# Kernel optimization log

Measured on AMD Instinct MI355X. Metric: run time of the kernel, lower is better.

The kernel has to match this reference:

```python
import jax, jax.numpy as jnp
import numpy as np
import math

C64 = jnp.complex64

def _fftconv_full(a, kern):
    # full linear convolution along last axis (complex), like scipy.signal.fftconvolve
    L = a.shape[-1] + kern.shape[0] - 1
    A = jnp.fft.fft(a, n=L, axis=-1)
    K = jnp.fft.fft(kern.astype(a.dtype), n=L)
    return jnp.fft.ifft(A * K, axis=-1)

def _centered_ifft(f):
    # out[shft] = ifft(f[shft]) * sqrt(N), shft = (arange(N)+fix(N/2)) % N
    N = f.shape[-1]
    shft = (np.arange(N) + int(np.fix(N / 2))) % N
    inv = np.argsort(shft)
    g = jnp.fft.ifft(f[..., shft], axis=-1) * math.sqrt(N)
    return g[..., inv].astype(f.dtype)

def _sincinterp(f):
    # zero-stuff by 2 then sinc-filter; returns length 2N-1 along last axis
    N = f.shape[-1]
    y = jnp.zeros(f.shape[:-1] + (2 * N - 1,), f.dtype).at[..., ::2].set(f)
    kern = jnp.asarray(np.sinc(np.arange(-(2 * N - 3), 2 * N - 2) / 2.0).astype(np.complex64))
    return _fftconv_full(y, kern)[..., 2 * N - 3: 4 * N - 4]

def _frft_chirp(f, a):
    # Ozaktas chirp-convolution discrete FrFT, valid for 0.5 <= a <= 1.5
    N = f.shape[-1]
    alpha = a * math.pi / 2
    tana2, sina = math.tan(alpha / 2), math.sin(alpha)
    fi = _sincinterp(f)                                   # [..., 2N-1]
    pad = jnp.zeros(f.shape[:-1] + (N - 1,), f.dtype)
    fp = jnp.concatenate([pad, fi, pad], axis=-1)         # [..., 4N-3]
    n = np.arange(-2 * N + 2, 2 * N - 1).astype(np.float64)
    chrp = jnp.asarray(np.exp(-1j * math.pi / N * tana2 / 4 * n ** 2).astype(np.complex64))
    fp = chrp * fp
    c = math.pi / N / sina / 4
    m = np.arange(-(4 * N - 4), 4 * N - 3).astype(np.float64)
    kern = jnp.asarray(np.exp(1j * c * m ** 2).astype(np.complex64))
    ret = _fftconv_full(fp, kern)[..., 4 * N - 4: 8 * N - 7] * math.sqrt(c / math.pi)
    ret = chrp * ret
    phase = np.complex64(np.exp(-1j * (1 - a) * math.pi / 4))
    return phase * ret[..., N - 1: 3 * N - 2: 2]          # [..., N]

def _frft_last(f, a):
    # torch branch logic for the a values used here: a=0.5 (fwd), a=-0.5 (inv)
    if a < 0.5:
        f = _centered_ifft(f)
        a = a + 1.0
    return _frft_chirp(f, a)

def _frft2d(x, a):
    t = _frft_last(x, a)                                  # rows: along W
    return jnp.swapaxes(_frft_last(jnp.swapaxes(t, -1, -2), a), -1, -2)  # cols: along H

def _c1x1(x, w, b=None):
    y = jnp.einsum('nchw,oc->nohw', x, w)
    return y if b is None else y + b[None, :, None, None]

def _c3x3(x, w, b):
    y = jax.lax.conv_general_dilated(x, w, (1, 1), 'SAME',
                                     dimension_numbers=('NCHW', 'OIHW', 'NCHW'))
    return y + b[None, :, None, None]

def _forward(x, conv1_w, mag_s_w, mag_s_b, mag_f_w, mag_f_b, mag_w, mag_b,
             pha_w, pha_b, conv_0_w, conv_0_b, conv_1_w, conv_1_b, conv2_w):
    angle = 0.5
    alpha = math.cos(angle * math.pi / 2)
    N, C, H, W = x.shape
    H1, W1 = int(H * alpha), int(W * alpha)
    x1 = _c1x1(x, conv1_w)                                # stride=1 -> downsample is identity
    C1, C0 = C // 4, C // 4 // 3
    x_0, x_05, x_1 = x1[:, :C0], x1[:, C0:C1 - C0], x1[:, C1 - C0:C1]
    h0, w0 = (H - H1) // 2, (W - W1) // 2
    mask1 = jnp.zeros((H, W), jnp.float32).at[h0:h0 + H1, w0:w0 + W1].set(1.0)
    mask2 = 1.0 - mask1
    # fractional Fourier branch
    Fre = _frft2d(x_05.astype(C64), angle)
    mag, pha = jnp.abs(Fre), jnp.angle(Fre)
    mag_out = _c1x1(_c3x3(mag * mask1, mag_s_w, mag_s_b) * mask1
                    + _c1x1(mag * mask2, mag_f_w, mag_f_b) * mask2, mag_w, mag_b)
    pha_out = _c1x1(pha, pha_w, pha_b)
    Fre_out = jax.lax.complex(mag_out * jnp.cos(pha_out), mag_out * jnp.sin(pha_out))
    ifrft = jnp.abs(_frft2d(Fre_out, -angle))
    # plain Fourier branch (conv_1 applied to both mag and pha, as in the source)
    fre = jnp.fft.rfft2(x_1)
    fm, fp = jnp.abs(fre), jnp.angle(fre)
    mo = _c1x1(fm, conv_1_w, conv_1_b)
    po = _c1x1(fp, conv_1_w, conv_1_b)
    x_1o = jnp.fft.irfft2(jax.lax.complex(mo * jnp.cos(po), mo * jnp.sin(po)), s=(H, W))
    x_0o = _c1x1(x_0, conv_0_w, conv_0_b)
    return _c1x1(jnp.concatenate([x_0o, ifrft, x_1o], axis=1), conv2_w)

def setup_inputs():
    key = jax.random.key(0)
    ks = jax.random.split(key, 16)
    N, C, H, W, Co = 4, 192, 128, 128, 192
    C1, C0 = C // 4, C // 4 // 3
    Cm = C1 - 2 * C0
    s = 0.05
    r = lambda k, sh: jax.random.normal(k, sh, jnp.float32)
    return {
        "x": r(ks[0], (N, C, H, W)),
        "conv1_w": r(ks[1], (C1, C)) * s,
        "mag_s_w": r(ks[2], (Cm, Cm, 3, 3)) * s, "mag_s_b": r(ks[3], (Cm,)) * s,
        "mag_f_w": r(ks[4], (Cm, Cm)) * s, "mag_f_b": r(ks[5], (Cm,)) * s,
        "mag_w": r(ks[6], (Cm, Cm)) * s, "mag_b": r(ks[7], (Cm,)) * s,
        "pha_w": r(ks[8], (Cm, Cm)) * s, "pha_b": r(ks[9], (Cm,)) * s,
        "conv_0_w": r(ks[10], (C0, C0)) * s, "conv_0_b": r(ks[11], (C0,)) * s,
        "conv_1_w": r(ks[12], (C0, C0)) * s, "conv_1_b": r(ks[13], (C0,)) * s,
        "conv2_w": r(ks[14], (Co, C1)) * s,
    }

def reference(x, conv1_w, mag_s_w, mag_s_b, mag_f_w, mag_f_b, mag_w, mag_b,
              pha_w, pha_b, conv_0_w, conv_0_b, conv_1_w, conv_1_b, conv2_w):
    return _forward(x, conv1_w, mag_s_w, mag_s_b, mag_f_w, mag_f_b, mag_w, mag_b,
                    pha_w, pha_b, conv_0_w, conv_0_b, conv_1_w, conv_1_b, conv2_w)
```

## Files before the change

kernel.cpp:

```cpp
#include <hip/hip_runtime.h>
#include <math.h>

#define PI_D 3.14159265358979323846
#define TWO_PI_F 6.2831853071795864f

__device__ __align__(16) float2 g_Mf [128*128];
__device__ __align__(16) float2 g_MfT[128*128];
__device__ __align__(16) float2 g_Mb [128*128];
__device__ __align__(16) float2 g_MbT[128*128];
__device__ __align__(16) float2 g_F  [128*128];
__device__ __align__(16) float2 g_IF [128*128];
__device__ __align__(16) float  g_x1 [4*48*16384];
__device__ __align__(16) float2 g_bufA[64*16384];
__device__ __align__(16) float2 g_bufB[64*16384];
__device__ __align__(16) float  g_mag[64*16384];
__device__ __align__(16) float  g_pha[64*16384];
__device__ __align__(16) float  g_m65[64*8320];
__device__ __align__(16) float  g_p65[64*8320];
__device__ __align__(16) float  g_t1 [64*16384];
__device__ __align__(16) float  g_t2 [64*16384];
__device__ __align__(16) float  g_t3 [64*8320];
__device__ __align__(16) float  g_t4 [64*8320];
__device__ __align__(16) float  g_cat[4*48*16384];

__device__ inline void build_A_body(int tid) {
    if (tid >= 128*128) return;
    int o = tid >> 7, m = tid & 127;
    const double chc = -PI_D/128.0 * tan(PI_D/8.0) * 0.25;
    const double c   =  PI_D/(512.0*sin(PI_D/4.0));
    const double inv2pi = 1.0/(2.0*PI_D);
    float sr, si;
    {
        int n1 = 2*m - 127, tt = 2*(o - m);
        double ang = chc*(double)(n1*n1) + c*(double)(tt*tt);
        double r = ang*inv2pi; r -= floor(r);
        float af = (float)(r*2.0*PI_D);
        float sn, cs; __sincosf(af, &sn, &cs);
        sr = cs; si = sn;
    }
    for (int j = 0; j < 127; ++j) {
        int q  = 2*j + 1;
        int n1 = q - 127, tt = 2*o - q, d = q - 2*m;
        double ang = chc*(double)(n1*n1) + c*(double)(tt*tt);
        double r = ang*inv2pi; r -= floor(r);
        float af = (float)(r*2.0*PI_D);
        float s = (((d-1)>>1) & 1) ? -2.0f : 2.0f;
        s /= (3.14159265358979f*(float)d);
        float sn, cs; __sincosf(af, &sn, &cs);
        sr += s*cs; si += s*sn;
    }
    int n2 = 2*o - 127;
    double ph = chc*(double)(n2*n2) - PI_D/8.0;
    double r = ph*inv2pi; r -= floor(r);
    float pf = (float)(r*2.0*PI_D);
    float scale = (float)sqrt(c/PI_D);
    float sn, cs; __sincosf(pf, &sn, &cs);
    float cr = cs*scale, ci = sn*scale;
    float2 v = make_float2(sr*cr - si*ci, sr*ci + si*cr);
    g_Mf[tid] = v;
    g_MfT[(m<<7) + o] = v;
    int p = (o*m) & 127;
    float ang2 = TWO_PI_F*(float)p/128.0f;
    float sn2, cs2; __sincosf(ang2, &sn2, &cs2);
    g_F[tid]  = make_float2(cs2, -sn2);
    g_IF[tid] = make_float2(cs2*0.0078125f, sn2*0.0078125f);
}

template<int LM>
__device__ inline void load_T4(float2* tr, const float* mp, const float* pp,
                               const float* Trl, int hh, int w4) {
    if (LM == 2) {
#pragma unroll
        for (int i = 0; i < 4; ++i) {
            int idx = (hh<<7) + w4 + i;
            float m = mp[idx], ph = pp[idx];
            float sn, cs; __sincosf(ph, &sn, &cs);
            tr[i] = make_float2(m*cs, m*sn);
        }
    } else {
#pragma unroll
        for (int i = 0; i < 4; ++i) {
            int w = w4 + i;
            int h2 = hh, w2 = w; float sg = 1.f;
            if (w >= 65) { h2 = (128 - hh) & 127; w2 = 128 - w; sg = -1.f; }
            int idx = h2*65 + w2;
            float m = mp[idx], ph = pp[idx];
            float sn, cs; __sincosf(ph, &sn, &cs);
            tr[i] = make_float2(m*cs, sg*m*sn);
        }
    }
}

__device__ inline void cfma(float2& a, float sx, float sy, float mx, float my) {
    a.x = fmaf(sx, mx, a.x); a.x = fmaf(-sy, my, a.x);
    a.y = fmaf(sx, my, a.y); a.y = fmaf(sy, mx, a.y);
}

template<int LM>
__device__ inline void rmul_body(const float2* __restrict__ MT, const float* __restrict__ Trl,
                                 const float* __restrict__ mp_, const float* __restrict__ pp_,
                                 float2* __restrict__ out, int cstart,
                                 int p, int r0, int t, float2* Ssh) {
    constexpr bool RS = (LM == 1);
    const float* Trp = nullptr; const float* mp = nullptr; const float* pp = nullptr;
    if (LM == 1) { int n = p >> 4, c = p & 15; Trp = Trl + ((long)(n*48 + cstart + c) << 14); }
    if (LM == 2) { mp = mp_ + ((long)p << 14); pp = pp_ + ((long)p << 14); }
    if (LM == 3) { mp = mp_ + (long)p*8320;   pp = pp_ + (long)p*8320; }
    int cq = t & 63, rp = t >> 6;
    const float* Tr_row[4];
    if (RS) {
#pragma unroll
        for (int i = 0; i < 4; ++i) {
            int ro = __builtin_amdgcn_readfirstlane((r0 + (rp<<2) + i) << 7);
            Tr_row[i] = Trp + ro;
        }
    } else {
        for (int u = t; u < 512; u += 256) {
            int row = u >> 5, w4 = (u & 31) << 2;
            float2 tr4[4];
            load_T4<LM>(tr4, mp, pp, Trp, r0 + row, w4);
            float4* d = (float4*)&Ssh[(row << 7) + w4];
            d[0] = make_float4(tr4[0].x, tr4[0].y, tr4[1].x, tr4[1].y);
            d[1] = make_float4(tr4[2].x, tr4[2].y, tr4[3].x, tr4[3].y);
        }
        __syncthreads();
    }
    float2 acc[4][2] = {};
#pragma unroll 8
    for (int k2 = 0; k2 < 64; ++k2) {
        int k = k2 << 1;
        float4 m0 = *(const float4*)&MT[(k << 7) + (cq<<1)];
        float4 m1 = *(const float4*)&MT[((k+1) << 7) + (cq<<1)];
        if (RS) {
            float2 sr4[4];
#pragma unroll
            for (int i = 0; i < 4; ++i)
                sr4[i] = *(const float2*)(Tr_row[i] + k);
#pragma unroll
            for (int i = 0; i < 4; ++i) {
                acc[i][0].x = fmaf(sr4[i].x, m0.x, acc[i][0].x);
                acc[i][0].y = fmaf(sr4[i].x, m0.y, acc[i][0].y);
                acc[i][1].x = fmaf(sr4[i].x, m0.z, acc[i][1].x);
                acc[i][1].y = fmaf(sr4[i].x, m0.w, acc[i][1].y);
                acc[i][0].x = fmaf(sr4[i].y, m1.x, acc[i][0].x);
                acc[i][0].y = fmaf(sr4[i].y, m1.y, acc[i][0].y);
                acc[i][1].x = fmaf(sr4[i].y, m1.z, acc[i][1].x);
                acc[i][1].y = fmaf(sr4[i].y, m1.w, acc[i][1].y);
            }
        } else {
            float4 s2[4];
#pragma unroll
            for (int i = 0; i < 4; ++i)
                s2[i] = *(const float4*)&Ssh[(((rp<<2)+i) << 7) + k];
#pragma unroll
            for (int i = 0; i < 4; ++i) {
                cfma(acc[i][0], s2[i].x, s2[i].y, m0.x, m0.y);
                cfma(acc[i][1], s2[i].x, s2[i].y, m0.z, m0.w);
                cfma(acc[i][0], s2[i].z, s2[i].w, m1.x, m1.y);
                cfma(acc[i][1], s2[i].z, s2[i].w, m1.z, m1.w);
            }
        }
    }
    long base = ((long)p << 14);
#pragma unroll
    for (int i = 0; i < 4; ++i) {
        float4* dst = (float4*)(out + base + ((long)(r0 + (rp<<2) + i) << 7) + (cq<<1));
        *dst = make_float4(acc[i][0].x, acc[i][0].y, acc[i][1].x, acc[i][1].y);
    }
}

template<int EPI>
__device__ inline void lmul_body(const float2* __restrict__ A, const float2* __restrict__ in,
                                 float* __restrict__ o1, float* __restrict__ o2, int coff,
                                 int p, int j0, int t) {
    const float2* T = in + ((long)p << 14);
    int cq = t & 63, rp = t >> 6;
    const float2* Arow[4];
#pragma unroll
    for (int i = 0; i < 4; ++i) {
        int ro = __builtin_amdgcn_readfirstlane((j0 + (rp<<2) + i) << 7);
        Arow[i] = A + ro;
    }
    float2 acc[4][2] = {};
#pragma unroll 8
    for (int k2 = 0; k2 < 64; ++k2) {
        int k = k2 << 1;
        float4 m0 = *(const float4*)&T[(k << 7) + (cq<<1)];
        float4 m1 = *(const float4*)&T[((k+1) << 7) + (cq<<1)];
        float4 s2[4];
#pragma unroll
        for (int i = 0; i < 4; ++i)
            s2[i] = *(const float4*)(Arow[i] + k);
#pragma unroll
        for (int i = 0; i < 4; ++i) {
            if (EPI == 3) {
                acc[i][0].x = fmaf(s2[i].x, m0.x, acc[i][0].x);
                acc[i][0].x = fmaf(-s2[i].y, m0.y, acc[i][0].x);
                acc[i][1].x = fmaf(s2[i].x, m0.z, acc[i][1].x);
                acc[i][1].x = fmaf(-s2[i].y, m0.w, acc[i][1].x);
                acc[i][0].x = fmaf(s2[i].z, m1.x, acc[i][0].x);
                acc[i][0].x = fmaf(-s2[i].w, m1.y, acc[i][0].x);
                acc[i][1].x = fmaf(s2[i].z, m1.z, acc[i][1].x);
                acc[i][1].x = fmaf(-s2[i].w, m1.w, acc[i][1].x);
            } else {
                cfma(acc[i][0], s2[i].x, s2[i].y, m0.x, m0.y);
                cfma(acc[i][1], s2[i].x, s2[i].y, m0.z, m0.w);
                cfma(acc[i][0], s2[i].z, s2[i].w, m1.x, m1.y);
                cfma(acc[i][1], s2[i].z, s2[i].w, m1.z, m1.w);
            }
        }
    }
#pragma unroll
    for (int i = 0; i < 4; ++i) {
        int jj = j0 + (rp<<2) + i;
        int ww0 = cq << 1;
        float2 v0 = acc[i][0], v1 = acc[i][1];
        if (EPI == 1) {
            long idx = ((long)p << 14) + ((long)jj << 7) + ww0;
            *(float2*)&o1[idx] = make_float2(sqrtf(v0.x*v0.x + v0.y*v0.y),
                                             sqrtf(v1.x*v1.x + v1.y*v1.y));
            *(float2*)&o2[idx] = make_float2(atan2f(v0.y, v0.x), atan2f(v1.y, v1.x));
        } else if (EPI == 2) {
            int n = p >> 4, c = p & 15;
            long idx = ((long)(n*48 + coff + c) << 14) + ((long)jj << 7) + ww0;
            *(float2*)&o1[idx] = make_float2(sqrtf(v0.x*v0.x + v0.y*v0.y),
                                             sqrtf(v1.x*v1.x + v1.y*v1.y));
        } else if (EPI == 3) {
            int n = p >> 4, c = p & 15;
            long idx = ((long)(n*48 + coff + c) << 14) + ((long)jj << 7) + ww0;
            *(float2*)&o1[idx] = make_float2(v0.x, v1.x);
        } else if (EPI == 4) {
            if (ww0 < 65) {
                long idx = (long)p*8320 + jj*65 + ww0;
                o1[idx] = sqrtf(v0.x*v0.x + v0.y*v0.y);
                o2[idx] = atan2f(v0.y, v0.x);
                if (ww0 + 1 < 65) {
                    o1[idx+1] = sqrtf(v1.x*v1.x + v1.y*v1.y);
                    o2[idx+1] = atan2f(v1.y, v1.x);
                }
            }
        }
    }
}

template<int LMA, int LMB>
__global__ __launch_bounds__(256, 4)
void k_rmul_dual(const float2* __restrict__ MTa, const float* __restrict__ TrlA,
                 const float* __restrict__ mpA, const float* __restrict__ ppA,
                 float2* __restrict__ outA, int cstartA,
                 const float2* __restrict__ MTb, const float* __restrict__ TrlB,
                 const float* __restrict__ mpB, const float* __restrict__ ppB,
                 float2* __restrict__ outB, int cstartB) {
    __shared__ __align__(16) float2 Ssh[(LMA == 1 && LMB == 1) ? 2 : 16*128];
    __shared__ float2 W[128];
    int bx = blockIdx.x, by = blockIdx.y, t = threadIdx.x;
    if (bx >= 128) {
        int b = (bx - 128)*8 + by;
        if (b < 64) {
            if (t < 128) {
                float ang = TWO_PI_F*(float)t/128.0f;
                float sn, cs; __sincosf(ang, &sn, &cs);
                float invs = 0.08838834764831845f;
                W[t] = make_float2(cs*invs, sn*invs);
            }
            __syncthreads();
            int tid = b*256 + t;
            int o = tid >> 7, m = tid & 127;
            float sr = 0.f, si = 0.f;
            for (int r = 0; r < 128; ++r) {
                float2 a = g_Mf[(o<<7) + r];
                int k = ((r+64)*(m+64)) & 127;
                float2 w = W[k];
                sr += a.x*w.x - a.y*w.y;
                si += a.x*w.y + a.y*w.x;
            }
            float2 v = make_float2(sr, si);
            g_Mb[tid] = v;
            g_MbT[(m<<7) + o] = v;
        }
        return;
    }
    int p = bx & 63, r0 = by << 4;
    if (bx < 64) rmul_body<LMA>(MTa, TrlA, mpA, ppA, outA, cstartA, p, r0, t, Ssh);
    else         rmul_body<LMB>(MTb, TrlB, mpB, ppB, outB, cstartB, p, r0, t, Ssh);
}

template<int EPIA, int EPIB>
__global__ __launch_bounds__(256, 4)
void k_lmul_dual(const float2* __restrict__ Aa, const float2* __restrict__ inA,
                 float* __restrict__ o1A, float* __restrict__ o2A, int coffA,
                 const float2* __restrict__ Ab, const float2* __restrict__ inB,
                 float* __restrict__ o1B, float* __restrict__ o2B, int coffB) {
    int bx = blockIdx.x, j0 = blockIdx.y << 4, t = threadIdx.x;
    int p = bx & 63;
    if (bx < 64) lmul_body<EPIA>(Aa, inA, o1A, o2A, coffA, p, j0, t);
    else         lmul_body<EPIB>(Ab, inB, o1B, o2B, coffB, p, j0, t);
}

template<int CIN, int COUT, int KSPLIT, int OSPLIT>
__device__ inline void wconv_body(const float* __restrict__ in, const float* __restrict__ wgt,
                                  const float* __restrict__ bias, float* __restrict__ out,
                                  int S, int Ctin, int cstart, int Ctout, int costart,
                                  int n, int sblk, float* red) {
    constexpr int OW = COUT / OSPLIT;
    constexpr int KC = CIN / KSPLIT;
    int t = threadIdx.x, lane = t & 63;
    int wv = __builtin_amdgcn_readfirstlane(t >> 6);
    int oq = wv / KSPLIT, kq = wv % KSPLIT;
    int s0 = sblk << 7;
    const float* inb = in + ((long)(n*Ctin + cstart + kq*KC))*S + s0 + (lane<<1);
    const float* wb  = wgt + (oq*OW)*CIN + kq*KC;
    float2 acc[OW];
#pragma unroll
    for (int j = 0; j < OW; ++j) acc[j] = make_float2(0.f, 0.f);
#pragma unroll 4
    for (int c = 0; c < KC; ++c) {
        float2 xv = *(const float2*)(inb + (long)c*S);
#pragma unroll
        for (int j = 0; j < OW; ++j) {
            float w = wb[j*CIN + c];
            acc[j].x = fmaf(w, xv.x, acc[j].x);
            acc[j].y = fmaf(w, xv.y, acc[j].y);
        }
    }
    if (KSPLIT == 1) {
#pragma unroll
        for (int j = 0; j < OW; ++j) {
            int o = oq*OW + j;
            float b = bias ? bias[o] : 0.f;
            *(float2*)(out + ((long)(n*Ctout + costart + o))*S + s0 + (lane<<1))
                = make_float2(acc[j].x + b, acc[j].y + b);
        }
    } else {
#pragma unroll
        for (int j = 0; j < OW; ++j) {
            int o = oq*OW + j;
            *(float2*)&red[((kq*COUT + o) << 7) + (lane<<1)] = acc[j];
        }
        __syncthreads();
        for (int idx = t; idx < COUT*64; idx += 256) {
            int o = idx >> 6, l2 = (idx & 63) << 1;
            float b = bias ? bias[o] : 0.f;
            float2 v = make_float2(b, b);
#pragma unroll
            for (int k2 = 0; k2 < KSPLIT; ++k2) {
                float2 r = *(const float2*)&red[((k2*COUT + o) << 7) + l2];
                v.x += r.x; v.y += r.y;
            }
            *(float2*)(out + ((long)(n*Ctout + costart + o))*S + s0 + l2) = v;
        }
    }
}

__global__ __launch_bounds__(256, 1)
void k_conv1_build(const float* __restrict__ x, const float* __restrict__ w,
                   float* __restrict__ x1) {
    __shared__ float red[2*48*128];
    if (blockIdx.z == 0) {
        wconv_body<192,48,2,2>(x, w, nullptr, x1, 16384, 192, 0, 48, 0,
                               blockIdx.y, blockIdx.x, red);
    } else {
        int b = blockIdx.y*gridDim.x + blockIdx.x;
        if (b < 64) build_A_body(b*256 + threadIdx.x);
    }
}

__global__ __launch_bounds__(256, 1)
void k_conv2(const float* __restrict__ in, const float* __restrict__ wgt,
             float* __restrict__ out) {
    __shared__ float red[1];
    wconv_body<48,192,1,4>(in, wgt, nullptr, out, 16384, 48, 0, 192, 0,
                           blockIdx.y, blockIdx.x, red);
}

__device__ inline void mix16b(const float* __restrict__ in, const float* __restrict__ w,
                              const float* __restrict__ b, float* __restrict__ out,
                              int Ctin, int S, int n, int s0base, int Slim) {
    int t = threadIdx.x, lane = t & 63;
    int wv = __builtin_amdgcn_readfirstlane(t >> 6);
    int oq = wv & 3, pg = wv >> 2;
    int s0 = s0base + (pg << 7);
    if (s0 >= Slim) return;
    const float* inb = in + ((long)(n*Ctin))*S + s0 + (lane<<1);
    float2 acc[4];
#pragma unroll
    for (int j = 0; j < 4; ++j) {
        float bb = b ? b[oq*4 + j] : 0.f;
        acc[j] = make_float2(bb, bb);
    }
#pragma unroll
    for (int half = 0; half < 2; ++half) {
        float2 xv[8];
#pragma unroll
        for (int c = 0; c < 8; ++c)
            xv[c] = *(const float2*)(inb + (long)(half*8 + c)*S);
#pragma unroll
        for (int c = 0; c < 8; ++c) {
#pragma unroll
            for (int j = 0; j < 4; ++j) {
                float ww = w[(oq*4 + j)*16 + half*8 + c];
                acc[j].x = fmaf(ww, xv[c].x, acc[j].x);
                acc[j].y = fmaf(ww, xv[c].y, acc[j].y);
            }
        }
    }
#pragma unroll
    for (int j = 0; j < 4; ++j) {
        int o = oq*4 + j;
        *(float2*)(out + ((long)(n*Ctin + o))*S + s0 + (lane<<1)) = acc[j];
    }
}

__device__ inline void maskconv_body(const float* __restrict__ mag, const float* __restrict__ ws3,
                                     const float* __restrict__ bs, const float* __restrict__ wf,
                                     const float* __restrict__ bf, const float* __restrict__ wm,
                                     const float* __restrict__ bm, float* __restrict__ out,
                                     int n, int tile, float* patch) {
    int h0 = (tile >> 3) << 4, w0 = (tile & 7) << 4;
    int t = threadIdx.x;
    const float* magn = mag + ((long)n << 18);
    for (int idx = t; idx < 16*324; idx += 1024) {
        int c = idx / 324, r = idx - c*324;
        int ph = r / 18, pw = r - ph*18;
        int gh = h0 - 1 + ph, gw = w0 - 1 + pw;
        float v = 0.f;
        if (gh >= 19 && gh < 109 && gw >= 19 && gw < 109)
            v = magn[(c<<14) + (gh<<7) + gw];
        patch[c*324 + r] = v;
    }
    __syncthreads();
    int oq = t >> 8, pix = t & 255;
    int ty = pix >> 4, tx = pix & 15;
    int h = h0 + ty, w = w0 + tx;
    bool in1 = (h >= 19 && h < 109 && w >= 19 && w < 109);
    unsigned long long bal = __ballot(in1);
    float res[4];
    if (bal != 0ull) {
        float acc[4];
#pragma unroll
        for (int j = 0; j < 4; ++j) acc[j] = bs[oq*4 + j];
        for (int c = 0; c < 16; ++c) {
            const float* pc = patch + c*324 + ty*18 + tx;
            const float* wc = ws3 + c*9;
#pragma unroll
            for (int dh = 0; dh < 3; ++dh) {
#pragma unroll
                for (int dw = 0; dw < 3; ++dw) {
                    float tap = pc[dh*18 + dw];
#pragma unroll
                    for (int j = 0; j < 4; ++j)
                        acc[j] = fmaf(wc[(oq*4 + j)*144 + dh*3 + dw], tap, acc[j]);
                }
            }
        }
#pragma unroll
        for (int j = 0; j < 4; ++j) res[j] = acc[j];
    }
    if (bal != ~0ull) {
        float acc2[4];
#pragma unroll
        for (int j = 0; j < 4; ++j) acc2[j] = bf[oq*4 + j];
#pragma unroll
        for (int half = 0; half < 2; ++half) {
            float xv[8];
#pragma unroll
            for (int c = 0; c < 8; ++c)
                xv[c] = magn[((half*8 + c)<<14) + (h<<7) + w];
#pragma unroll
            for (int c = 0; c < 8; ++c)
#pragma unroll
                for (int j = 0; j < 4; ++j)
                    acc2[j] = fmaf(wf[(oq*4 + j)*16 + half*8 + c], xv[c], acc2[j]);
        }
        if (!in1) {
#pragma unroll
            for (int j = 0; j < 4; ++j) res[j] = acc2[j];
        }
    }
    __syncthreads();
    float* resl = patch;
#pragma unroll
    for (int j = 0; j < 4; ++j) resl[(oq*4 + j)*256 + pix] = res[j];
    __syncthreads();
    float rr[16];
#pragma unroll
    for (int o = 0; o < 16; ++o) rr[o] = resl[o*256 + pix];
#pragma unroll
    for (int j = 0; j < 4; ++j) {
        int o2 = oq*4 + j;
        float a = bm[o2];
#pragma unroll
        for (int o = 0; o < 16; ++o)
            a = fmaf(wm[o2*16 + o], rr[o], a);
        out[((long)((n<<4) + o2) << 14) + (h << 7) + w] = a;
    }
}

__global__ __launch_bounds__(1024, 8)
void k_point(const float* __restrict__ mag, const float* __restrict__ ws3,
             const float* __restrict__ bs, const float* __restrict__ wf,
             const float* __restrict__ bf, const float* __restrict__ wm,
             const float* __restrict__ bm, float* __restrict__ t2,
             const float* __restrict__ pha, const float* __restrict__ pw,
             const float* __restrict__ pb, float* __restrict__ t1,
             const float* __restrict__ x1, const float* __restrict__ c0w,
             const float* __restrict__ c0b, float* __restrict__ cat,
             const float* __restrict__ m65, const float* __restrict__ p65,
             const float* __restrict__ c1w, const float* __restrict__ c1b,
             float* __restrict__ t3, float* __restrict__ t4) {
    __shared__ float patch[16*324];
    int b = blockIdx.x;
    if (b < 256) {
        maskconv_body(mag, ws3, bs, wf, bf, wm, bm, t2, b >> 6, b & 63, patch);
    } else if (b < 384) {
        int i = b - 256;
        mix16b(pha, pw, pb, t1, 16, 16384, i >> 5, (i & 31) << 9, 16384);
    } else if (b < 512) {
        int i = b - 384;
        mix16b(x1, c0w, c0b, cat, 48, 16384, i >> 5, (i & 31) << 9, 16384);
    } else if (b < 580) {
        int i = b - 512;
        mix16b(m65, c1w, c1b, t3, 16, 8320, i / 17, (i % 17) << 9, 8320);
    } else {
        int i = b - 580;
        mix16b(p65, c1w, c1b, t4, 16, 8320, i / 17, (i % 17) << 9, 8320);
    }
}

extern "C" void kernel_launch(void* const* d_in, const int* in_sizes, int n_in,
                              void* d_out, int out_size, void* d_ws, size_t ws_size,
                              hipStream_t stream) {
    (void)in_sizes; (void)n_in; (void)out_size; (void)d_ws; (void)ws_size;
    const float* x        = (const float*)d_in[0];
    const float* conv1_w  = (const float*)d_in[1];
    const float* mag_s_w  = (const float*)d_in[2];
    const float* mag_s_b  = (const float*)d_in[3];
    const float* mag_f_w  = (const float*)d_in[4];
    const float* mag_f_b  = (const float*)d_in[5];
    const float* mag_w_   = (const float*)d_in[6];
    const float* mag_b_   = (const float*)d_in[7];
    const float* pha_w_   = (const float*)d_in[8];
    const float* pha_b_   = (const float*)d_in[9];
    const float* conv_0_w = (const float*)d_in[10];
    const float* conv_0_b = (const float*)d_in[11];
    const float* conv_1_w = (const float*)d_in[12];
    const float* conv_1_b = (const float*)d_in[13];
    const float* conv2_w  = (const float*)d_in[14];
    float* outp = (float*)d_out;

    float2 *Mf, *MfT, *Mb, *MbT, *Fm, *IFm, *bufA, *bufB;
    float *x1, *mag, *pha, *m65, *p65, *t1, *t2, *t3, *t4, *cat;
    hipGetSymbolAddress((void**)&Mf,   HIP_SYMBOL(g_Mf));
    hipGetSymbolAddress((void**)&MfT,  HIP_SYMBOL(g_MfT));
    hipGetSymbolAddress((void**)&Mb,   HIP_SYMBOL(g_Mb));
    hipGetSymbolAddress((void**)&MbT,  HIP_SYMBOL(g_MbT));
    hipGetSymbolAddress((void**)&Fm,   HIP_SYMBOL(g_F));
    hipGetSymbolAddress((void**)&IFm,  HIP_SYMBOL(g_IF));
    hipGetSymbolAddress((void**)&bufA, HIP_SYMBOL(g_bufA));
    hipGetSymbolAddress((void**)&bufB, HIP_SYMBOL(g_bufB));
    hipGetSymbolAddress((void**)&x1,   HIP_SYMBOL(g_x1));
    hipGetSymbolAddress((void**)&mag,  HIP_SYMBOL(g_mag));
    hipGetSymbolAddress((void**)&pha,  HIP_SYMBOL(g_pha));
    hipGetSymbolAddress((void**)&m65,  HIP_SYMBOL(g_m65));
    hipGetSymbolAddress((void**)&p65,  HIP_SYMBOL(g_p65));
    hipGetSymbolAddress((void**)&t1,   HIP_SYMBOL(g_t1));
    hipGetSymbolAddress((void**)&t2,   HIP_SYMBOL(g_t2));
    hipGetSymbolAddress((void**)&t3,   HIP_SYMBOL(g_t3));
    hipGetSymbolAddress((void**)&t4,   HIP_SYMBOL(g_t4));
    hipGetSymbolAddress((void**)&cat,  HIP_SYMBOL(g_cat));

    dim3 bt(256, 1, 1);

    k_conv1_build<<<dim3(128,4,2), bt, 0, stream>>>(x, conv1_w, x1);

    k_rmul_dual<1,1><<<dim3(136,8), bt, 0, stream>>>(
        MfT, x1, nullptr, nullptr, bufA, 16,
        Fm,  x1, nullptr, nullptr, bufB, 32);

    k_lmul_dual<1,4><<<dim3(128,8), bt, 0, stream>>>(
        Mf, bufA, mag, pha, 0,
        Fm, bufB, m65, p65, 0);

    k_point<<<648, dim3(1024,1,1), 0, stream>>>(mag, mag_s_w, mag_s_b, mag_f_w, mag_f_b,
                                                mag_w_, mag_b_, t2,
                                                pha, pha_w_, pha_b_, t1,
                                                x1, conv_0_w, conv_0_b, cat,
                                                m65, p65, conv_1_w, conv_1_b, t3, t4);

    k_rmul_dual<2,3><<<dim3(128,8), bt, 0, stream>>>(
        MbT, nullptr, t2, t1, bufA, 0,
        IFm, nullptr, t3, t4, bufB, 0);

    k_lmul_dual<2,3><<<dim3(128,8), bt, 0, stream>>>(
        Mb,  bufA, cat, nullptr, 16,
        IFm, bufB, cat, nullptr, 32);

    k_conv2<<<dim3(128,4), bt, 0, stream>>>(cat, conv2_w, outp);
}
```

Baseline: 306.3 us.

## Drop K-split reduction in 1x1 convs and split conv2 outputs across grid

The 1x1 convolution body no longer splits the input-channel reduction across waves with an LDS reduction. Each wave now owns 12 outputs and loops over all inputs. conv2 is launched with twice the blocks, each computing 96 of the 192 output channels, which halves the per-thread accumulators. Launch bounds go up to 4 blocks per CU to raise occupancy. The trade-off is a longer per-wave reduction in conv1 and input activations being reread twice in conv2.

```diff
diff --git a/kernel.cpp b/kernel.cpp
--- a/kernel.cpp
+++ b/kernel.cpp
@@ -297,24 +297,22 @@
     else         lmul_body<EPIB>(Ab, inB, o1B, o2B, coffB, p, j0, t);
 }
 
-template<int CIN, int COUT, int KSPLIT, int OSPLIT>
+template<int CIN, int COUT, int OSPLIT>
 __device__ inline void wconv_body(const float* __restrict__ in, const float* __restrict__ wgt,
                                   const float* __restrict__ bias, float* __restrict__ out,
                                   int S, int Ctin, int cstart, int Ctout, int costart,
-                                  int n, int sblk, float* red) {
+                                  int n, int sblk) {
     constexpr int OW = COUT / OSPLIT;
-    constexpr int KC = CIN / KSPLIT;
     int t = threadIdx.x, lane = t & 63;
-    int wv = __builtin_amdgcn_readfirstlane(t >> 6);
-    int oq = wv / KSPLIT, kq = wv % KSPLIT;
+    int oq = __builtin_amdgcn_readfirstlane(t >> 6);
     int s0 = sblk << 7;
-    const float* inb = in + ((long)(n*Ctin + cstart + kq*KC))*S + s0 + (lane<<1);
-    const float* wb  = wgt + (oq*OW)*CIN + kq*KC;
+    const float* inb = in + ((long)(n*Ctin + cstart))*S + s0 + (lane<<1);
+    const float* wb  = wgt + (oq*OW)*CIN;
     float2 acc[OW];
 #pragma unroll
     for (int j = 0; j < OW; ++j) acc[j] = make_float2(0.f, 0.f);
 #pragma unroll 4
-    for (int c = 0; c < KC; ++c) {
+    for (int c = 0; c < CIN; ++c) {
         float2 xv = *(const float2*)(inb + (long)c*S);
 #pragma unroll
         for (int j = 0; j < OW; ++j) {
@@ -323,54 +321,33 @@
             acc[j].y = fmaf(w, xv.y, acc[j].y);
         }
     }
-    if (KSPLIT == 1) {
-#pragma unroll
-        for (int j = 0; j < OW; ++j) {
-            int o = oq*OW + j;
-            float b = bias ? bias[o] : 0.f;
-            *(float2*)(out + ((long)(n*Ctout + costart + o))*S + s0 + (lane<<1))
-                = make_float2(acc[j].x + b, acc[j].y + b);
-        }
-    } else {
-#pragma unroll
-        for (int j = 0; j < OW; ++j) {
-            int o = oq*OW + j;
-            *(float2*)&red[((kq*COUT + o) << 7) + (lane<<1)] = acc[j];
-        }
-        __syncthreads();
-        for (int idx = t; idx < COUT*64; idx += 256) {
-            int o = idx >> 6, l2 = (idx & 63) << 1;
-            float b = bias ? bias[o] : 0.f;
-            float2 v = make_float2(b, b);
-#pragma unroll
-            for (int k2 = 0; k2 < KSPLIT; ++k2) {
-                float2 r = *(const float2*)&red[((k2*COUT + o) << 7) + l2];
-                v.x += r.x; v.y += r.y;
-            }
-            *(float2*)(out + ((long)(n*Ctout + costart + o))*S + s0 + l2) = v;
-        }
-    }
-}
-
-__global__ __launch_bounds__(256, 1)
+#pragma unroll
+    for (int j = 0; j < OW; ++j) {
+        int o = oq*OW + j;
+        float b = bias ? bias[o] : 0.f;
+        *(float2*)(out + ((long)(n*Ctout + costart + o))*S + s0 + (lane<<1))
+            = make_float2(acc[j].x + b, acc[j].y + b);
+    }
+}
+
+__global__ __launch_bounds__(256, 4)
 void k_conv1_build(const float* __restrict__ x, const float* __restrict__ w,
                    float* __restrict__ x1) {
-    __shared__ float red[2*48*128];
     if (blockIdx.z == 0) {
-        wconv_body<192,48,2,2>(x, w, nullptr, x1, 16384, 192, 0, 48, 0,
-                               blockIdx.y, blockIdx.x, red);
+        wconv_body<192,48,4>(x, w, nullptr, x1, 16384, 192, 0, 48, 0,
+                             blockIdx.y, blockIdx.x);
     } else {
         int b = blockIdx.y*gridDim.x + blockIdx.x;
         if (b < 64) build_A_body(b*256 + threadIdx.x);
     }
 }
 
-__global__ __launch_bounds__(256, 1)
+__global__ __launch_bounds__(256, 4)
 void k_conv2(const float* __restrict__ in, const float* __restrict__ wgt,
              float* __restrict__ out) {
-    __shared__ float red[1];
-    wconv_body<48,192,1,4>(in, wgt, nullptr, out, 16384, 48, 0, 192, 0,
-                           blockIdx.y, blockIdx.x, red);
+    int z = blockIdx.z;
+    wconv_body<48,96,4>(in, wgt + z*96*48, nullptr, out, 16384, 48, 0, 192, z*96,
+                        blockIdx.y, blockIdx.x);
 }
 
 __device__ inline void mix16b(const float* __restrict__ in, const float* __restrict__ w,
@@ -595,5 +572,5 @@
         Mb,  bufA, cat, nullptr, 16,
         IFm, bufB, cat, nullptr, 32);
 
-    k_conv2<<<dim3(128,4), bt, 0, stream>>>(cat, conv2_w, outp);
-}
+    k_conv2<<<dim3(128,4,2), bt, 0, stream>>>(cat, conv2_w, outp);
+}
```

New measurement: 313.6 us. 1.02x slower.
